# Kernel tuning notes

Measured on AMD Instinct MI355X. Metric: run time of the kernel, lower is better.

## Reference

```python
import jax, jax.numpy as jnp
import numpy as np

BS, D, H = 65536, 768, 12
DK = D // H // 2  # 32
EPS = 1e-6

def setup_inputs() -> dict:
    key = jax.random.key(0)
    ks = jax.random.split(key, 4)
    scale = 1.0 / np.sqrt(D)
    return {
        "x": jax.random.normal(ks[0], (BS, D), dtype=jnp.float32),
        "Wq": jax.random.normal(ks[1], (D, D), dtype=jnp.float32) * scale,
        "Wk": jax.random.normal(ks[2], (D, D), dtype=jnp.float32) * scale,
        "Wv": jax.random.normal(ks[3], (D, D), dtype=jnp.float32) * scale,
        "gamma": jnp.ones((D,), dtype=jnp.float32),
        "beta": jnp.zeros((D,), dtype=jnp.float32),
    }

def reference(x, Wq, Wk, Wv, gamma, beta):
    bs = x.shape[0]
    # LayerNorm (eps=1e-6)
    mu = jnp.mean(x, axis=-1, keepdims=True)
    var = jnp.mean(jnp.square(x - mu), axis=-1, keepdims=True)
    xn = (x - mu) / jnp.sqrt(var + EPS) * gamma + beta
    # QKV projections (nn.Linear, no bias: y = x @ W.T), split feature dim as (h, 2, d_k)
    q = (xn @ Wq.T).reshape(bs, H, 2, DK)
    k = (xn @ Wk.T).reshape(bs, H, 2, DK)
    v = (xn @ Wv.T).reshape(bs, H, 2, DK)
    # tiny 2x2 attention per head
    scores = jnp.einsum('bhpd,bhqd->bhpq', q, k) / np.sqrt(DK)
    attn = jax.nn.softmax(scores, axis=-1)
    out = jnp.einsum('bhpq,bhqd->bhpd', attn, v).reshape(bs, D)
    return out + x
```

## Files before the change

kernel.cpp:

```cpp
#include <hip/hip_runtime.h>

typedef _Float16 f16;
typedef _Float16 f16x8 __attribute__((ext_vector_type(8)));
typedef float f32x16 __attribute__((ext_vector_type(16)));

#define BS 65536
#define D 768
#define H 12
#define RB 128
#define NBLK ((BS / RB) * H)
#define W_ELEMS ((size_t)D * D)
#define XN_ELEMS ((size_t)BS * D)

typedef const __attribute__((address_space(1))) void gvoid_t;
typedef __attribute__((address_space(3))) void lvoid_t;


__global__ __launch_bounds__(256, 4) void ln_kernel(const float* __restrict__ x,
                                                    const float* __restrict__ gamma,
                                                    const float* __restrict__ beta,
                                                    f16* __restrict__ xp) {
  __shared__ float sSum[16][17], sSq[16][17];
  const int tid = threadIdx.x;
  const int r  = tid & 15;
  const int sg = tid >> 4;
  const size_t R = (size_t)blockIdx.x * 16 + r;
  const float4* xs = (const float4*)(x + R * D + sg * 48);
  float4 v[12];
  float sum = 0.f, sq = 0.f;
#pragma unroll
  for (int j = 0; j < 12; ++j) {
    v[j] = xs[j];
    sum += (v[j].x + v[j].y) + (v[j].z + v[j].w);
    sq  += v[j].x * v[j].x + v[j].y * v[j].y + v[j].z * v[j].z + v[j].w * v[j].w;
  }
  sSum[sg][r] = sum; sSq[sg][r] = sq;
  __syncthreads();
  float ts = 0.f, tq = 0.f;
#pragma unroll
  for (int k = 0; k < 16; ++k) { ts += sSum[k][r]; tq += sSq[k][r]; }
  const float mu   = ts * (1.0f / D);
  const float rstd = rsqrtf(tq * (1.0f / D) - mu * mu + 1e-6f);

  const float4* g4 = (const float4*)(gamma + sg * 48);
  const float4* b4 = (const float4*)(beta  + sg * 48);
  const int rb12 = (int)(R >> 5) * 12;
  const int r31  = (int)(R & 31);
#pragma unroll
  for (int jj = 0; jj < 6; ++jj) {
    const int k = sg * 48 + jj * 8;
    float4 g0 = g4[2 * jj], g1 = g4[2 * jj + 1];
    float4 b0 = b4[2 * jj], b1 = b4[2 * jj + 1];
    float4 u0 = v[2 * jj],  u1 = v[2 * jj + 1];
    f16x8 o;
    o[0] = (f16)((u0.x - mu) * rstd * g0.x + b0.x);
    o[1] = (f16)((u0.y - mu) * rstd * g0.y + b0.y);
    o[2] = (f16)((u0.z - mu) * rstd * g0.z + b0.z);
    o[3] = (f16)((u0.w - mu) * rstd * g0.w + b0.w);
    o[4] = (f16)((u1.x - mu) * rstd * g1.x + b1.x);
    o[5] = (f16)((u1.y - mu) * rstd * g1.y + b1.y);
    o[6] = (f16)((u1.z - mu) * rstd * g1.z + b1.z);
    o[7] = (f16)((u1.w - mu) * rstd * g1.w + b1.w);
    size_t addr = ((size_t)(rb12 + (k >> 6))) * 2048 + ((k >> 4) & 3) * 512
                + ((k >> 3) & 1) * 256 + r31 * 8;
    *(f16x8*)(xp + addr) = o;
  }
}

__global__ __launch_bounds__(256, 4) void wconv_kernel(const float* __restrict__ Wq,
                                                       const float* __restrict__ Wk,
                                                       const float* __restrict__ Wv,
                                                       f16* __restrict__ wf) {
  int b = blockIdx.x;
  int m = b / 288;
  size_t e = ((size_t)(b % 288) * 256 + threadIdx.x) * 8;
  const float* src = (m == 0 ? Wq : (m == 1 ? Wk : Wv)) + e;
  float4 v0 = *(const float4*)src;
  float4 v1 = *(const float4*)(src + 4);
  f16x8 o;
  o[0] = (f16)v0.x; o[1] = (f16)v0.y; o[2] = (f16)v0.z; o[3] = (f16)v0.w;
  o[4] = (f16)v1.x; o[5] = (f16)v1.y; o[6] = (f16)v1.z; o[7] = (f16)v1.w;
  *(f16x8*)(wf + (size_t)m * W_ELEMS + e) = o;
}

__global__ __launch_bounds__(256, 3) void qkv_attn_kernel(const f16* __restrict__ xp,
                                                          const f16* __restrict__ wf,
                                                          const float* __restrict__ x,
                                                          float* __restrict__ out) {
  __shared__ f16 sB[2][192 * 64] __attribute__((aligned(16)));

  const int tid  = threadIdx.x;
  const int wave = tid >> 6;
  const int lane = tid & 63;
  const int l31  = lane & 31;
  const int hi   = lane >> 5;

  int bid = blockIdx.x;
  int my  = (bid & 7) * (NBLK / 8) + (bid >> 3);
  int rb  = my / H;
  int h   = my % H;

  const int ri = lane >> 3;
  const int ci = lane & 7;

  unsigned boffs[6];
#pragma unroll
  for (int o = 0; o < 6; ++o) {
    int n = wave * 48 + o * 8 + ri;
    boffs[o] = (unsigned)((n >> 6) * (int)W_ELEMS + (h * 64 + (n & 63)) * D + ((ci ^ ri) * 8));
  }

  const int q7 = l31 & 7;
  int coff[4];
#pragma unroll
  for (int s = 0; s < 4; ++s) coff[s] = l31 * 64 + (((s * 2 + hi) ^ q7) * 8);

  const f16* ap = xp + ((size_t)(rb * 4 + wave) * 12) * 2048 + hi * 256 + l31 * 8;

#define STAGE(KO, BUF)                                                                   \
  {                                                                                      \
    _Pragma("unroll") for (int o = 0; o < 6; ++o) {                                      \
      __builtin_amdgcn_global_load_lds((gvoid_t*)(wf + boffs[o] + (KO) * 64),            \
                                       (lvoid_t*)(&sB[BUF][(wave * 48 + o * 8) * 64]),   \
                                       16, 0, 0);                                        \
    }                                                                                    \
  }

  STAGE(0, 0);

  f32x16 acc[6];
#pragma unroll
  for (int t = 0; t < 6; ++t)
#pragma unroll
    for (int i = 0; i < 16; ++i) acc[t][i] = 0.f;

#pragma unroll
  for (int ko = 0; ko < 12; ++ko) {
    const int cur = ko & 1;

    f16x8 a0 = *(const f16x8*)(ap + ko * 2048);
    f16x8 a1 = *(const f16x8*)(ap + ko * 2048 + 512);
    f16x8 a2 = *(const f16x8*)(ap + ko * 2048 + 1024);
    f16x8 a3 = *(const f16x8*)(ap + ko * 2048 + 1536);
    __builtin_amdgcn_sched_barrier(0);
    if (ko < 11) STAGE(ko + 1, cur ^ 1);
    __builtin_amdgcn_sched_barrier(0);
    if (ko < 11) asm volatile("s_waitcnt vmcnt(10)" ::: "memory");
    else         asm volatile("s_waitcnt vmcnt(4)" ::: "memory");
    __builtin_amdgcn_sched_barrier(0);
    __builtin_amdgcn_s_barrier();

    __builtin_amdgcn_s_setprio(1);
    {
      f16x8 b;
#pragma unroll
      for (int t = 0; t < 6; ++t) {
        b = *(const f16x8*)(&sB[cur][coff[0] + t * 2048]);
        acc[t] = __builtin_amdgcn_mfma_f32_32x32x16_f16(a0, b, acc[t], 0, 0, 0);
      }
#pragma unroll
      for (int t = 0; t < 6; ++t) {
        b = *(const f16x8*)(&sB[cur][coff[1] + t * 2048]);
        acc[t] = __builtin_amdgcn_mfma_f32_32x32x16_f16(a1, b, acc[t], 0, 0, 0);
      }
#pragma unroll
      for (int t = 0; t < 6; ++t) {
        b = *(const f16x8*)(&sB[cur][coff[2] + t * 2048]);
        acc[t] = __builtin_amdgcn_mfma_f32_32x32x16_f16(a2, b, acc[t], 0, 0, 0);
      }
#pragma unroll
      for (int t = 0; t < 6; ++t) {
        b = *(const f16x8*)(&sB[cur][coff[3] + t * 2048]);
        acc[t] = __builtin_amdgcn_mfma_f32_32x32x16_f16(a3, b, acc[t], 0, 0, 0);
      }
    }
    __builtin_amdgcn_s_setprio(0);

    if (ko < 11) {
      asm volatile("s_waitcnt lgkmcnt(0)" ::: "memory");
      __builtin_amdgcn_sched_barrier(0);
      __builtin_amdgcn_s_barrier();
    }
  }

  {
    const size_t grow0 = (size_t)rb * RB + wave * 32;
    const float scale = 0.17677669529663687f;
#pragma unroll
    for (int g = 0; g < 16; ++g) {
      float q0 = acc[0][g], q1 = acc[1][g];
      float k0 = acc[2][g], k1 = acc[3][g];
      float s00 = q0 * k0, s01 = q0 * k1, s10 = q1 * k0, s11 = q1 * k1;
#pragma unroll
      for (int d2 = 1; d2 <= 16; d2 <<= 1) {
        s00 += __shfl_xor(s00, d2, 64);
        s01 += __shfl_xor(s01, d2, 64);
        s10 += __shfl_xor(s10, d2, 64);
        s11 += __shfl_xor(s11, d2, 64);
      }
      s00 *= scale; s01 *= scale; s10 *= scale; s11 *= scale;
      float mx0 = fmaxf(s00, s01);
      float e00 = __expf(s00 - mx0), e01 = __expf(s01 - mx0);
      float r0 = 1.0f / (e00 + e01);
      float a00 = e00 * r0, a01 = e01 * r0;
      float mx1 = fmaxf(s10, s11);
      float e10 = __expf(s10 - mx1), e11 = __expf(s11 - mx1);
      float r1 = 1.0f / (e10 + e11);
      float a10 = e10 * r1, a11 = e11 * r1;

      int row_w = (g & 3) + 8 * (g >> 2) + 4 * hi;
      const float* xq = x   + (grow0 + row_w) * D + h * 64 + l31;
      float*       op = out + (grow0 + row_w) * D + h * 64 + l31;
      float v0 = acc[4][g], v1 = acc[5][g];
      op[0]  = a00 * v0 + a01 * v1 + xq[0];
      op[32] = a10 * v0 + a11 * v1 + xq[32];
    }
  }
#undef STAGE
}

extern "C" void kernel_launch(void* const* d_in, const int* in_sizes, int n_in,
                              void* d_out, int out_size, void* d_ws, size_t ws_size,
                              hipStream_t stream) {
  const float* x     = (const float*)d_in[0];
  const float* Wq    = (const float*)d_in[1];
  const float* Wk    = (const float*)d_in[2];
  const float* Wv    = (const float*)d_in[3];
  const float* gamma = (const float*)d_in[4];
  const float* beta  = (const float*)d_in[5];
  float* out = (float*)d_out;
  (void)in_sizes; (void)n_in; (void)out_size; (void)ws_size;

  f16* xp = (f16*)d_ws;
  f16* wf = xp + XN_ELEMS;

  ln_kernel<<<dim3(BS / 16), dim3(256), 0, stream>>>(x, gamma, beta, xp);
  wconv_kernel<<<dim3(864), dim3(256), 0, stream>>>(Wq, Wk, Wv, wf);
  qkv_attn_kernel<<<dim3(NBLK), dim3(256), 0, stream>>>(xp, wf, x, out);
}
```

Baseline: 643.8 us.

## Retile QKV GEMM into 2x2 wave grid and stage LayerNorm output through LDS

```diff
diff --git a/kernel.cpp b/kernel.cpp
--- a/kernel.cpp
+++ b/kernel.cpp
@@ -2,6 +2,7 @@
 
 typedef _Float16 f16;
 typedef _Float16 f16x8 __attribute__((ext_vector_type(8)));
+typedef _Float16 f16x4 __attribute__((ext_vector_type(4)));
 typedef float f32x16 __attribute__((ext_vector_type(16)));
 
 #define BS 65536
@@ -11,59 +12,71 @@
 #define NBLK ((BS / RB) * H)
 #define W_ELEMS ((size_t)D * D)
 #define XN_ELEMS ((size_t)BS * D)
+#define LNS 776
 
 typedef const __attribute__((address_space(1))) void gvoid_t;
 typedef __attribute__((address_space(3))) void lvoid_t;
 
 
-__global__ __launch_bounds__(256, 4) void ln_kernel(const float* __restrict__ x,
-                                                    const float* __restrict__ gamma,
-                                                    const float* __restrict__ beta,
-                                                    f16* __restrict__ xp) {
-  __shared__ float sSum[16][17], sSq[16][17];
+__global__ __launch_bounds__(256) void ln_kernel(const float* __restrict__ x,
+                                                 const float* __restrict__ gamma,
+                                                 const float* __restrict__ beta,
+                                                 f16* __restrict__ xp) {
+  __shared__ f16 sX[32][LNS];
   const int tid = threadIdx.x;
-  const int r  = tid & 15;
-  const int sg = tid >> 4;
-  const size_t R = (size_t)blockIdx.x * 16 + r;
-  const float4* xs = (const float4*)(x + R * D + sg * 48);
-  float4 v[12];
-  float sum = 0.f, sq = 0.f;
-#pragma unroll
-  for (int j = 0; j < 12; ++j) {
-    v[j] = xs[j];
-    sum += (v[j].x + v[j].y) + (v[j].z + v[j].w);
-    sq  += v[j].x * v[j].x + v[j].y * v[j].y + v[j].z * v[j].z + v[j].w * v[j].w;
-  }
-  sSum[sg][r] = sum; sSq[sg][r] = sq;
+  const int wave = tid >> 6, lane = tid & 63;
+  const size_t rowbase = (size_t)blockIdx.x * 32;
+
+  const float4* g4 = (const float4*)(gamma + lane * 12);
+  const float4* b4 = (const float4*)(beta  + lane * 12);
+  float4 g0 = g4[0], g1 = g4[1], g2 = g4[2];
+  float4 b0 = b4[0], b1 = b4[1], b2 = b4[2];
+
+#pragma unroll
+  for (int r8 = 0; r8 < 8; ++r8) {
+    const int row = wave * 8 + r8;
+    const float4* xr = (const float4*)(x + (rowbase + row) * D + lane * 12);
+    float4 v0 = xr[0], v1 = xr[1], v2 = xr[2];
+    float sum = (v0.x + v0.y) + (v0.z + v0.w) + (v1.x + v1.y) + (v1.z + v1.w)
+              + (v2.x + v2.y) + (v2.z + v2.w);
+    float sq = v0.x*v0.x + v0.y*v0.y + v0.z*v0.z + v0.w*v0.w
+             + v1.x*v1.x + v1.y*v1.y + v1.z*v1.z + v1.w*v1.w
+             + v2.x*v2.x + v2.y*v2.y + v2.z*v2.z + v2.w*v2.w;
+#pragma unroll
+    for (int d2 = 1; d2 <= 32; d2 <<= 1) {
+      sum += __shfl_xor(sum, d2, 64);
+      sq  += __shfl_xor(sq,  d2, 64);
+    }
+    const float mu   = sum * (1.0f / D);
+    const float rstd = rsqrtf(sq * (1.0f / D) - mu * mu + 1e-6f);
+    f16* sw = &sX[row][lane * 12];
+    f16x4 o;
+    o[0] = (f16)((v0.x - mu) * rstd * g0.x + b0.x);
+    o[1] = (f16)((v0.y - mu) * rstd * g0.y + b0.y);
+    o[2] = (f16)((v0.z - mu) * rstd * g0.z + b0.z);
+    o[3] = (f16)((v0.w - mu) * rstd * g0.w + b0.w);
+    *(f16x4*)(sw) = o;
+    o[0] = (f16)((v1.x - mu) * rstd * g1.x + b1.x);
+    o[1] = (f16)((v1.y - mu) * rstd * g1.y + b1.y);
+    o[2] = (f16)((v1.z - mu) * rstd * g1.z + b1.z);
+    o[3] = (f16)((v1.w - mu) * rstd * g1.w + b1.w);
+    *(f16x4*)(sw + 4) = o;
+    o[0] = (f16)((v2.x - mu) * rstd * g2.x + b2.x);
+    o[1] = (f16)((v2.y - mu) * rstd * g2.y + b2.y);
+    o[2] = (f16)((v2.z - mu) * rstd * g2.z + b2.z);
+    o[3] = (f16)((v2.w - mu) * rstd * g2.w + b2.w);
+    *(f16x4*)(sw + 8) = o;
+  }
   __syncthreads();
-  float ts = 0.f, tq = 0.f;
-#pragma unroll
-  for (int k = 0; k < 16; ++k) { ts += sSum[k][r]; tq += sSq[k][r]; }
-  const float mu   = ts * (1.0f / D);
-  const float rstd = rsqrtf(tq * (1.0f / D) - mu * mu + 1e-6f);
-
-  const float4* g4 = (const float4*)(gamma + sg * 48);
-  const float4* b4 = (const float4*)(beta  + sg * 48);
-  const int rb12 = (int)(R >> 5) * 12;
-  const int r31  = (int)(R & 31);
-#pragma unroll
-  for (int jj = 0; jj < 6; ++jj) {
-    const int k = sg * 48 + jj * 8;
-    float4 g0 = g4[2 * jj], g1 = g4[2 * jj + 1];
-    float4 b0 = b4[2 * jj], b1 = b4[2 * jj + 1];
-    float4 u0 = v[2 * jj],  u1 = v[2 * jj + 1];
-    f16x8 o;
-    o[0] = (f16)((u0.x - mu) * rstd * g0.x + b0.x);
-    o[1] = (f16)((u0.y - mu) * rstd * g0.y + b0.y);
-    o[2] = (f16)((u0.z - mu) * rstd * g0.z + b0.z);
-    o[3] = (f16)((u0.w - mu) * rstd * g0.w + b0.w);
-    o[4] = (f16)((u1.x - mu) * rstd * g1.x + b1.x);
-    o[5] = (f16)((u1.y - mu) * rstd * g1.y + b1.y);
-    o[6] = (f16)((u1.z - mu) * rstd * g1.z + b1.z);
-    o[7] = (f16)((u1.w - mu) * rstd * g1.w + b1.w);
-    size_t addr = ((size_t)(rb12 + (k >> 6))) * 2048 + ((k >> 4) & 3) * 512
-                + ((k >> 3) & 1) * 256 + r31 * 8;
-    *(f16x8*)(xp + addr) = o;
+  f16* base = xp + (size_t)blockIdx.x * 24576;
+  const int s    = (tid >> 6) & 3;
+  const int half = (tid >> 5) & 1;
+  const int row  = tid & 31;
+#pragma unroll
+  for (int i = 0; i < 12; ++i) {
+    const int k = i * 64 + s * 16 + half * 8;
+    f16x8 v = *(const f16x8*)(&sX[row][k]);
+    *(f16x8*)(base + i * 2048 + tid * 8) = v;
   }
 }
 
@@ -94,6 +107,8 @@
   const int lane = tid & 63;
   const int l31  = lane & 31;
   const int hi   = lane >> 5;
+  const int wr   = wave >> 1;
+  const int wc   = wave & 1;
 
   int bid = blockIdx.x;
   int my  = (bid & 7) * (NBLK / 8) + (bid >> 3);
@@ -114,8 +129,12 @@
   int coff[4];
 #pragma unroll
   for (int s = 0; s < 4; ++s) coff[s] = l31 * 64 + (((s * 2 + hi) ^ q7) * 8);
-
-  const f16* ap = xp + ((size_t)(rb * 4 + wave) * 12) * 2048 + hi * 256 + l31 * 8;
+  const int tb0 = (wc ? 1 : 0) * 2048;
+  const int tb1 = (wc ? 4 : 2) * 2048;
+  const int tb2 = (wc ? 5 : 3) * 2048;
+
+  const f16* ap0 = xp + ((size_t)(rb * 4 + wr * 2) * 12) * 2048 + hi * 256 + l31 * 8;
+  const f16* ap1 = ap0 + 12 * 2048;
 
 #define STAGE(KO, BUF)                                                                   \
   {                                                                                      \
@@ -128,51 +147,44 @@
 
   STAGE(0, 0);
 
-  f32x16 acc[6];
-#pragma unroll
-  for (int t = 0; t < 6; ++t)
-#pragma unroll
-    for (int i = 0; i < 16; ++i) acc[t][i] = 0.f;
+  f32x16 acc[3][2];
+#pragma unroll
+  for (int t = 0; t < 3; ++t)
+#pragma unroll
+    for (int rt = 0; rt < 2; ++rt)
+#pragma unroll
+      for (int i = 0; i < 16; ++i) acc[t][rt][i] = 0.f;
 
 #pragma unroll
   for (int ko = 0; ko < 12; ++ko) {
     const int cur = ko & 1;
 
-    f16x8 a0 = *(const f16x8*)(ap + ko * 2048);
-    f16x8 a1 = *(const f16x8*)(ap + ko * 2048 + 512);
-    f16x8 a2 = *(const f16x8*)(ap + ko * 2048 + 1024);
-    f16x8 a3 = *(const f16x8*)(ap + ko * 2048 + 1536);
+    f16x8 a0[4], a1[4];
+#pragma unroll
+    for (int s = 0; s < 4; ++s) {
+      a0[s] = *(const f16x8*)(ap0 + ko * 2048 + s * 512);
+      a1[s] = *(const f16x8*)(ap1 + ko * 2048 + s * 512);
+    }
     __builtin_amdgcn_sched_barrier(0);
     if (ko < 11) STAGE(ko + 1, cur ^ 1);
     __builtin_amdgcn_sched_barrier(0);
-    if (ko < 11) asm volatile("s_waitcnt vmcnt(10)" ::: "memory");
-    else         asm volatile("s_waitcnt vmcnt(4)" ::: "memory");
+    if (ko < 11) asm volatile("s_waitcnt vmcnt(14)" ::: "memory");
+    else         asm volatile("s_waitcnt vmcnt(8)" ::: "memory");
     __builtin_amdgcn_sched_barrier(0);
     __builtin_amdgcn_s_barrier();
 
     __builtin_amdgcn_s_setprio(1);
-    {
-      f16x8 b;
-#pragma unroll
-      for (int t = 0; t < 6; ++t) {
-        b = *(const f16x8*)(&sB[cur][coff[0] + t * 2048]);
-        acc[t] = __builtin_amdgcn_mfma_f32_32x32x16_f16(a0, b, acc[t], 0, 0, 0);
-      }
-#pragma unroll
-      for (int t = 0; t < 6; ++t) {
-        b = *(const f16x8*)(&sB[cur][coff[1] + t * 2048]);
-        acc[t] = __builtin_amdgcn_mfma_f32_32x32x16_f16(a1, b, acc[t], 0, 0, 0);
-      }
-#pragma unroll
-      for (int t = 0; t < 6; ++t) {
-        b = *(const f16x8*)(&sB[cur][coff[2] + t * 2048]);
-        acc[t] = __builtin_amdgcn_mfma_f32_32x32x16_f16(a2, b, acc[t], 0, 0, 0);
-      }
-#pragma unroll
-      for (int t = 0; t < 6; ++t) {
-        b = *(const f16x8*)(&sB[cur][coff[3] + t * 2048]);
-        acc[t] = __builtin_amdgcn_mfma_f32_32x32x16_f16(a3, b, acc[t], 0, 0, 0);
-      }
+#pragma unroll
+    for (int s = 0; s < 4; ++s) {
+      f16x8 b0 = *(const f16x8*)(&sB[cur][tb0 + coff[s]]);
+      f16x8 b1 = *(const f16x8*)(&sB[cur][tb1 + coff[s]]);
+      f16x8 b2 = *(const f16x8*)(&sB[cur][tb2 + coff[s]]);
+      acc[0][0] = __builtin_amdgcn_mfma_f32_32x32x16_f16(a0[s], b0, acc[0][0], 0, 0, 0);
+      acc[0][1] = __builtin_amdgcn_mfma_f32_32x32x16_f16(a1[s], b0, acc[0][1], 0, 0, 0);
+      acc[1][0] = __builtin_amdgcn_mfma_f32_32x32x16_f16(a0[s], b1, acc[1][0], 0, 0, 0);
+      acc[1][1] = __builtin_amdgcn_mfma_f32_32x32x16_f16(a1[s], b1, acc[1][1], 0, 0, 0);
+      acc[2][0] = __builtin_amdgcn_mfma_f32_32x32x16_f16(a0[s], b2, acc[2][0], 0, 0, 0);
+      acc[2][1] = __builtin_amdgcn_mfma_f32_32x32x16_f16(a1[s], b2, acc[2][1], 0, 0, 0);
     }
     __builtin_amdgcn_s_setprio(0);
 
@@ -183,37 +195,64 @@
     }
   }
 
-  {
-    const size_t grow0 = (size_t)rb * RB + wave * 32;
-    const float scale = 0.17677669529663687f;
-#pragma unroll
-    for (int g = 0; g < 16; ++g) {
-      float q0 = acc[0][g], q1 = acc[1][g];
-      float k0 = acc[2][g], k1 = acc[3][g];
-      float s00 = q0 * k0, s01 = q0 * k1, s10 = q1 * k0, s11 = q1 * k1;
-#pragma unroll
-      for (int d2 = 1; d2 <= 16; d2 <<= 1) {
-        s00 += __shfl_xor(s00, d2, 64);
-        s01 += __shfl_xor(s01, d2, 64);
-        s10 += __shfl_xor(s10, d2, 64);
-        s11 += __shfl_xor(s11, d2, 64);
+  f16*   sK0 = &sB[0][0];
+  f16*   sK1 = &sB[0][4096];
+  float* sS  = (float*)&sB[0][8192];
+  const float scale = 0.17677669529663687f;
+
+  if (wc == 0) {
+#pragma unroll
+    for (int rt = 0; rt < 2; ++rt) {
+#pragma unroll
+      for (int g = 0; g < 16; ++g) {
+        const int row = wr * 64 + rt * 32 + (g & 3) + 8 * (g >> 2) + 4 * hi;
+        float q0 = acc[0][rt][g], k0 = acc[1][rt][g], k1 = acc[2][rt][g];
+        float t00 = q0 * k0, t01 = q0 * k1;
+#pragma unroll
+        for (int d2 = 1; d2 <= 16; d2 <<= 1) {
+          t00 += __shfl_xor(t00, d2, 64);
+          t01 += __shfl_xor(t01, d2, 64);
+        }
+        sK0[row * 32 + l31] = (f16)k0;
+        sK1[row * 32 + l31] = (f16)k1;
+        if (l31 == 0) { sS[row * 2] = t00 * scale; sS[row * 2 + 1] = t01 * scale; }
       }
-      s00 *= scale; s01 *= scale; s10 *= scale; s11 *= scale;
-      float mx0 = fmaxf(s00, s01);
-      float e00 = __expf(s00 - mx0), e01 = __expf(s01 - mx0);
-      float r0 = 1.0f / (e00 + e01);
-      float a00 = e00 * r0, a01 = e01 * r0;
-      float mx1 = fmaxf(s10, s11);
-      float e10 = __expf(s10 - mx1), e11 = __expf(s11 - mx1);
-      float r1 = 1.0f / (e10 + e11);
-      float a10 = e10 * r1, a11 = e11 * r1;
-
-      int row_w = (g & 3) + 8 * (g >> 2) + 4 * hi;
-      const float* xq = x   + (grow0 + row_w) * D + h * 64 + l31;
-      float*       op = out + (grow0 + row_w) * D + h * 64 + l31;
-      float v0 = acc[4][g], v1 = acc[5][g];
-      op[0]  = a00 * v0 + a01 * v1 + xq[0];
-      op[32] = a10 * v0 + a11 * v1 + xq[32];
+    }
+  }
+  __syncthreads();
+  if (wc == 1) {
+#pragma unroll
+    for (int rt = 0; rt < 2; ++rt) {
+#pragma unroll
+      for (int g = 0; g < 16; ++g) {
+        const int row = wr * 64 + rt * 32 + (g & 3) + 8 * (g >> 2) + 4 * hi;
+        float q1 = acc[0][rt][g];
+        float k0 = (float)sK0[row * 32 + l31];
+        float k1 = (float)sK1[row * 32 + l31];
+        float t10 = q1 * k0, t11 = q1 * k1;
+#pragma unroll
+        for (int d2 = 1; d2 <= 16; d2 <<= 1) {
+          t10 += __shfl_xor(t10, d2, 64);
+          t11 += __shfl_xor(t11, d2, 64);
+        }
+        float s00 = sS[row * 2], s01 = sS[row * 2 + 1];
+        float s10 = t10 * scale, s11 = t11 * scale;
+        float mx0 = fmaxf(s00, s01);
+        float e00 = __expf(s00 - mx0), e01 = __expf(s01 - mx0);
+        float r0 = 1.0f / (e00 + e01);
+        float a00 = e00 * r0, a01 = e01 * r0;
+        float mx1 = fmaxf(s10, s11);
+        float e10 = __expf(s10 - mx1), e11 = __expf(s11 - mx1);
+        float r1 = 1.0f / (e10 + e11);
+        float a10 = e10 * r1, a11 = e11 * r1;
+
+        float v0 = acc[1][rt][g], v1 = acc[2][rt][g];
+        const size_t grow = (size_t)rb * RB + row;
+        const float* xq = x   + grow * D + h * 64 + l31;
+        float*       op = out + grow * D + h * 64 + l31;
+        op[0]  = a00 * v0 + a01 * v1 + xq[0];
+        op[32] = a10 * v0 + a11 * v1 + xq[32];
+      }
     }
   }
 #undef STAGE
@@ -234,7 +273,7 @@
   f16* xp = (f16*)d_ws;
   f16* wf = xp + XN_ELEMS;
 
-  ln_kernel<<<dim3(BS / 16), dim3(256), 0, stream>>>(x, gamma, beta, xp);
+  ln_kernel<<<dim3(BS / 32), dim3(256), 0, stream>>>(x, gamma, beta, xp);
   wconv_kernel<<<dim3(864), dim3(256), 0, stream>>>(Wq, Wk, Wv, wf);
   qkv_attn_kernel<<<dim3(NBLK), dim3(256), 0, stream>>>(xp, wf, x, out);
 }
```

After: 1.179 ms. 83.2% more time.
